# Performance work log

Hardware: AMD Instinct MI355X
Metric: run time of the kernel (lower is better)

Reference implementation:

```python
import jax, jax.numpy as jnp
import numpy as np
from jax import lax

B, C, H, W = 4, 64, 384, 384


def setup_inputs() -> dict:
    key = jax.random.key(0)
    ks = jax.random.split(key, 9)
    s = 1.0 / np.sqrt(C)
    inp = {
        "x": jax.random.normal(ks[0], (B, C, H, W), dtype=jnp.float32),
        "W1": jax.random.normal(ks[1], (C, C), dtype=jnp.float32) * s,
        "b1": jax.random.normal(ks[2], (C,), dtype=jnp.float32) * 0.01,
        "W2": jax.random.normal(ks[3], (C, C), dtype=jnp.float32) * s,
        "b2": jax.random.normal(ks[4], (C,), dtype=jnp.float32) * 0.01,
        "W4": jax.random.normal(ks[5], (C, C), dtype=jnp.float32) * s,
        "b4": jax.random.normal(ks[6], (C,), dtype=jnp.float32) * 0.01,
        "W5": jax.random.normal(ks[7], (C, C), dtype=jnp.float32) * s,
        "b5": jax.random.normal(ks[8], (C,), dtype=jnp.float32) * 0.01,
    }
    return inp


def _lin(Wm, b, t):
    # 1x1 Conv1d == per-position linear: t is (B, C, L)
    return jnp.einsum('oc,bcl->bol', Wm, t) + b[None, :, None]


def reference(x, W1, b1, W2, b2, W4, b4, W5, b5):
    # ---- vertical (top->down) scan over height ----
    rows = jnp.moveaxis(x, 2, 0)          # (H, B, C, W)
    row0 = rows[0]                        # row 0 untouched (no relu in loop 1)

    def vstep(prev, xi):
        new = jax.nn.relu(_lin(W1, b1, xi) + _lin(W2, b2, prev))
        return new, new

    _, vrest = lax.scan(vstep, row0, rows[1:])
    hs = jnp.concatenate([row0[None], vrest], axis=0)   # (H, B, C, W)
    hs = jnp.moveaxis(hs, 0, 2)                          # (B, C, H, W)

    # ---- horizontal (left->right) scan over width ----
    cols = jnp.moveaxis(hs, 3, 0)         # (W, B, C, H)
    col0 = jax.nn.relu(cols[0])           # relu applied to column 0 as well

    def hstep(prev, cj):
        new = jax.nn.relu(_lin(W4, b4, cj) + _lin(W5, b5, prev))
        return new, new

    _, hrest = lax.scan(hstep, col0, cols[1:])
    hse = jnp.concatenate([col0[None], hrest], axis=0)   # (W, B, C, H)
    out = jnp.moveaxis(hse, 0, 3)                        # (B, C, H, W)
    return out
```

## Files before the change

kernel.cpp:

```cpp
#include <hip/hip_runtime.h>


#define C64 64
#define S   384

typedef float v2f __attribute__((ext_vector_type(2)));

static __device__ __forceinline__ v2f mk2(float a, float b) {
    v2f r; r.x = a; r.y = b; return r;
}

#define LOADRB16(SRC)                                                         \
    float4 rb[16];                                                            \
    {                                                                         \
        const float4* vq4_ = (const float4*)(SRC);                            \
        _Pragma("unroll")                                                     \
        for (int i_ = 0; i_ < 16; ++i_) rb[i_] = vq4_[i_];                    \
    }
#define MATVEC16(DST, WREG, INIT)                                             \
    float DST;                                                                \
    {                                                                         \
        v2f a0 = mk2((INIT), 0.f), a1 = mk2(0.f,0.f),                         \
            a2v = mk2(0.f,0.f),    a3 = mk2(0.f,0.f);                         \
        _Pragma("unroll")                                                     \
        for (int i_ = 0; i_ < 8; ++i_) {                                      \
            float4 r0 = rb[2*i_], r1 = rb[2*i_+1];                            \
            a0  = __builtin_elementwise_fma(WREG[4*i_+0], mk2(r0.x,r0.y), a0);\
            a1  = __builtin_elementwise_fma(WREG[4*i_+1], mk2(r0.z,r0.w), a1);\
            a2v = __builtin_elementwise_fma(WREG[4*i_+2], mk2(r1.x,r1.y), a2v);\
            a3  = __builtin_elementwise_fma(WREG[4*i_+3], mk2(r1.z,r1.w), a3);\
        }                                                                     \
        v2f sv = (a0 + a1) + (a2v + a3);                                      \
        DST = sv.x + sv.y;                                                    \
    }

#define MATVEC_H(DST, WREG, SRC, INIT)                                        \
    float DST;                                                                \
    {                                                                         \
        const float4* vq4_ = (const float4*)(SRC);                            \
        v2f a0 = mk2((INIT), 0.f), a1 = mk2(0.f,0.f),                         \
            a2v = mk2(0.f,0.f),    a3 = mk2(0.f,0.f);                         \
        _Pragma("unroll")                                                     \
        for (int h_ = 0; h_ < 2; ++h_) {                                      \
            float4 rb8[8];                                                    \
            _Pragma("unroll")                                                 \
            for (int i_ = 0; i_ < 8; ++i_) rb8[i_] = vq4_[8*h_ + i_];         \
            _Pragma("unroll")                                                 \
            for (int i_ = 0; i_ < 4; ++i_) {                                  \
                float4 r0 = rb8[2*i_], r1 = rb8[2*i_+1];                      \
                a0  = __builtin_elementwise_fma(WREG[16*h_+4*i_+0],           \
                                                mk2(r0.x,r0.y), a0);          \
                a1  = __builtin_elementwise_fma(WREG[16*h_+4*i_+1],           \
                                                mk2(r0.z,r0.w), a1);          \
                a2v = __builtin_elementwise_fma(WREG[16*h_+4*i_+2],           \
                                                mk2(r1.x,r1.y), a2v);         \
                a3  = __builtin_elementwise_fma(WREG[16*h_+4*i_+3],           \
                                                mk2(r1.z,r1.w), a3);          \
            }                                                                 \
        }                                                                     \
        v2f sv = (a0 + a1) + (a2v + a3);                                      \
        DST = sv.x + sv.y;                                                    \
    }

#define LOADW(WSEL)                                                           \
    {                                                                         \
        const float4* P4_ = (const float4*)((WSEL) + o * C64);                \
        _Pragma("unroll")                                                     \
        for (int i_ = 0; i_ < 16; ++i_) {                                     \
            float4 u_ = P4_[i_];                                              \
            wr2[2*i_+0] = mk2(u_.x, u_.y);                                    \
            wr2[2*i_+1] = mk2(u_.z, u_.w);                                    \
        }                                                                     \
        _Pragma("unroll")                                                     \
        for (int i_ = 0; i_ < 32; ++i_) asm volatile("" : "+v"(wr2[i_]));     \
    }

__global__ __launch_bounds__(256, 4)
void prelin_kernel(const float* __restrict__ X, float* __restrict__ A,
                   const float* __restrict__ W, const float* __restrict__ bx,
                   const float* __restrict__ by)
{
    __shared__ float os[C64][68];
    const int p  = blockIdx.x;
    const int q0 = blockIdx.y * 64;
    const int b  = blockIdx.z;
    const int t  = threadIdx.x, wid = t >> 6, l = t & 63;
    const int q  = q0 + l;
    const int o0 = __builtin_amdgcn_readfirstlane(wid * 16);

    if (p == 0) {
        const int tb = ((b * C64 + o0) * S) * S + q;
#pragma unroll
        for (int j = 0; j < 16; ++j)
            os[l][o0 + j] = X[tb + j * S * S];
    } else {
        v2f acc[16];
#pragma unroll
        for (int j = 0; j < 16; ++j) acc[j] = mk2(0.f, 0.f);
#pragma unroll
        for (int cb = 0; cb < 2; ++cb) {
            v2f vin[16];
            const int tb = ((b * C64 + cb * 32) * S + p) * S + q;
#pragma unroll
            for (int i = 0; i < 16; ++i)
                vin[i] = mk2(X[tb + (2*i) * S*S], X[tb + (2*i+1) * S*S]);
#pragma unroll
            for (int j = 0; j < 16; ++j) {
                const v2f* wr = (const v2f*)(W + (o0 + j) * C64 + cb * 32);
#pragma unroll
                for (int i = 0; i < 16; ++i)
                    acc[j] = __builtin_elementwise_fma(wr[i], vin[i], acc[j]);
            }
        }
#pragma unroll
        for (int j = 0; j < 16; ++j)
            os[l][o0 + j] = acc[j].x + acc[j].y + bx[o0 + j] + by[o0 + j];
    }
    __syncthreads();

#pragma unroll
    for (int kk = 0; kk < 4; ++kk) {
        const int qq = 16 * kk + (l >> 2);
        const int oo = 16 * wid + 4 * (l & 3);
        *(float4*)(A + (((b*S + (q0+qq))*S + p) * C64 + oo)) =
            *(const float4*)&os[qq][oo];
    }
}

__global__ __launch_bounds__(64, 2)
void scan1_kernel(const float* __restrict__ A1, float* __restrict__ hsT,
                  const float* __restrict__ W2)
{
    __shared__ float vs[2][C64];
    const int o = threadIdx.x;
    const int g = blockIdx.x, b = g / S, w = g - b * S;

    v2f wr2[32];
    LOADW(W2)

    const int abase = ((b * S + w) * S) * C64 + o;
    const int sb    = (b * S * S + w) * C64 + o;

    float v0 = A1[abase];
    vs[1][o] = v0;
    hsT[sb]  = v0;
    float af[8];
#pragma unroll
    for (int h = 1; h <= 8; ++h) af[h & 7] = A1[abase + h * C64];
    __builtin_amdgcn_wave_barrier();

#define S1STEP(H, PAR)                                                        \
    {                                                                         \
        LOADRB16(&vs[PAR][0])                                                 \
        MATVEC16(s_, wr2, af[(H) & 7])                                        \
        float vnew = fmaxf(s_, 0.0f);                                         \
        vs[(PAR) ^ 1][o] = vnew;                                              \
        hsT[sb + (H) * (S * C64)] = vnew;                                     \
        int hn = (H) + 8; hn = (hn > S - 1) ? (S - 1) : hn;                   \
        af[(H) & 7] = A1[abase + hn * C64];                                   \
        __builtin_amdgcn_wave_barrier();                                      \
    }

    for (int h = 1; h < S - 1; h += 2) { S1STEP(h, 1) S1STEP(h + 1, 0) }
    S1STEP(S - 1, 1)
#undef S1STEP
}

__global__ __launch_bounds__(128, 2)
void scan2_kernel(const float* __restrict__ hsT, float* __restrict__ out,
                  const float* __restrict__ W4, const float* __restrict__ b4,
                  const float* __restrict__ b5, const float* __restrict__ W5)
{
    __shared__ float xr[32][C64];
    __shared__ float xs[2][32][C64];
    __shared__ float vs[2][C64];

    const int t = threadIdx.x, wid = t >> 6, o = t & 63;
    const int g = blockIdx.x, b = g / S, hr = g - b * S;

    const int hbase = ((b * S + hr) * S) * C64 + o;
    const int outb  = ((b * C64 + o) * S + hr) * S;

    v2f wr2[32];
    { const float* Wsel = (wid == 0) ? W5 : W4; LOADW(Wsel) }

    float bias = 0.f;
    if (wid == 1) bias = b4[o] + b5[o];
    if (wid == 0) vs[1][o] = 0.f;
    float ob[16];
    __syncthreads();

    for (int ph = 0; ph < 13; ++ph) {
        if (wid == 1) {
            if (ph < 12) {
                const int k = ph, cb = k & 1, wb = 32 * k;
                float xg[32];
#pragma unroll
                for (int i = 0; i < 32; ++i)
                    xg[i] = hsT[hbase + (wb + i) * C64];
#pragma unroll
                for (int i = 0; i < 32; ++i)
                    xr[i][o] = xg[i];
                __builtin_amdgcn_wave_barrier();
                for (int i = 0; i < 32; ++i) {
                    MATVEC_H(a_, wr2, &xr[i][0], bias)
                    float val = (k == 0 && i == 0) ? xg[0] : a_;
                    xs[cb][i][o] = val;
                }
            }
        } else {
            if (ph >= 1) {
                const int m = ph - 1, cb = m & 1, wb = 32 * m;
                const float* xsrow = &xs[cb][0][0];
#define P2STEP(HALF, I)                                                       \
    {                                                                         \
        MATVEC_H(s_, wr2, &vs[((I) + 1) & 1][0],                              \
                 xsrow[((HALF) * 16 + (I)) * C64 + o])                        \
        float vnew = fmaxf(s_, 0.0f);                                         \
        vs[(I) & 1][o] = vnew;                                                \
        ob[I] = vnew;                                                         \
        __builtin_amdgcn_wave_barrier();                                      \
    }
#define STORE16(BASE)                                                         \
    {                                                                         \
        float4 s0 = {ob[0],  ob[1],  ob[2],  ob[3]};                          \
        float4 s1 = {ob[4],  ob[5],  ob[6],  ob[7]};                          \
        float4 s2 = {ob[8],  ob[9],  ob[10], ob[11]};                         \
        float4 s3 = {ob[12], ob[13], ob[14], ob[15]};                         \
        float4* pp = (float4*)(out + outb + (BASE));                          \
        pp[0] = s0; pp[1] = s1; pp[2] = s2; pp[3] = s3;                       \
    }
                for (int half = 0; half < 2; ++half) {
                    P2STEP(half,  0) P2STEP(half,  1) P2STEP(half,  2)
                    P2STEP(half,  3) P2STEP(half,  4) P2STEP(half,  5)
                    P2STEP(half,  6) P2STEP(half,  7) P2STEP(half,  8)
                    P2STEP(half,  9) P2STEP(half, 10) P2STEP(half, 11)
                    P2STEP(half, 12) P2STEP(half, 13) P2STEP(half, 14)
                    P2STEP(half, 15)
                    STORE16(wb + 16 * half)
                }
#undef P2STEP
#undef STORE16
            }
        }
        __syncthreads();
    }
}

extern "C" void kernel_launch(void* const* d_in, const int* in_sizes, int n_in,
                              void* d_out, int out_size, void* d_ws, size_t ws_size,
                              hipStream_t stream) {
    const float* x  = (const float*)d_in[0];
    const float* W1 = (const float*)d_in[1];
    const float* b1 = (const float*)d_in[2];
    const float* W2 = (const float*)d_in[3];
    const float* b2 = (const float*)d_in[4];
    const float* W4 = (const float*)d_in[5];
    const float* b4 = (const float*)d_in[6];
    const float* W5 = (const float*)d_in[7];
    const float* b5 = (const float*)d_in[8];
    float* out = (float*)d_out;
    float* ws  = (float*)d_ws;

    prelin_kernel<<<dim3(S, 6, 4), dim3(256), 0, stream>>>(x, out, W1, b1, b2);
    scan1_kernel<<<dim3(4 * S), dim3(64), 0, stream>>>(out, ws, W2);
    scan2_kernel<<<dim3(4 * S), dim3(128), 0, stream>>>(ws, out, W4, b4, b5, W5);
}
```

Baseline: 743.3 us.

## Fuse W4 input projection into vertical scan and simplify horizontal scan kernel

The vertical scan kernel now also applies W4 (plus b4+b5) to each new row state, reusing the same LDS-loaded vector for both matvecs, and writes the precomputed horizontal input projection to the workspace. Column 0 keeps the raw relu'd value. The horizontal scan kernel drops its producer/consumer two-wave pipeline with LDS staging and block-wide syncs, becoming a single-wave recurrence that only does the W5 matvec with a 16-deep register prefetch. This takes the W4 matvec off the second kernel's critical path, at the cost of doubling register weight storage and FMA work in the first scan.

```diff
diff --git a/kernel.cpp b/kernel.cpp
--- a/kernel.cpp
+++ b/kernel.cpp
@@ -10,69 +10,17 @@
     v2f r; r.x = a; r.y = b; return r;
 }
 
-#define LOADRB16(SRC)                                                         \
-    float4 rb[16];                                                            \
-    {                                                                         \
-        const float4* vq4_ = (const float4*)(SRC);                            \
-        _Pragma("unroll")                                                     \
-        for (int i_ = 0; i_ < 16; ++i_) rb[i_] = vq4_[i_];                    \
-    }
-#define MATVEC16(DST, WREG, INIT)                                             \
-    float DST;                                                                \
-    {                                                                         \
-        v2f a0 = mk2((INIT), 0.f), a1 = mk2(0.f,0.f),                         \
-            a2v = mk2(0.f,0.f),    a3 = mk2(0.f,0.f);                         \
-        _Pragma("unroll")                                                     \
-        for (int i_ = 0; i_ < 8; ++i_) {                                      \
-            float4 r0 = rb[2*i_], r1 = rb[2*i_+1];                            \
-            a0  = __builtin_elementwise_fma(WREG[4*i_+0], mk2(r0.x,r0.y), a0);\
-            a1  = __builtin_elementwise_fma(WREG[4*i_+1], mk2(r0.z,r0.w), a1);\
-            a2v = __builtin_elementwise_fma(WREG[4*i_+2], mk2(r1.x,r1.y), a2v);\
-            a3  = __builtin_elementwise_fma(WREG[4*i_+3], mk2(r1.z,r1.w), a3);\
-        }                                                                     \
-        v2f sv = (a0 + a1) + (a2v + a3);                                      \
-        DST = sv.x + sv.y;                                                    \
-    }
-
-#define MATVEC_H(DST, WREG, SRC, INIT)                                        \
-    float DST;                                                                \
-    {                                                                         \
-        const float4* vq4_ = (const float4*)(SRC);                            \
-        v2f a0 = mk2((INIT), 0.f), a1 = mk2(0.f,0.f),                         \
-            a2v = mk2(0.f,0.f),    a3 = mk2(0.f,0.f);                         \
-        _Pragma("unroll")                                                     \
-        for (int h_ = 0; h_ < 2; ++h_) {                                      \
-            float4 rb8[8];                                                    \
-            _Pragma("unroll")                                                 \
-            for (int i_ = 0; i_ < 8; ++i_) rb8[i_] = vq4_[8*h_ + i_];         \
-            _Pragma("unroll")                                                 \
-            for (int i_ = 0; i_ < 4; ++i_) {                                  \
-                float4 r0 = rb8[2*i_], r1 = rb8[2*i_+1];                      \
-                a0  = __builtin_elementwise_fma(WREG[16*h_+4*i_+0],           \
-                                                mk2(r0.x,r0.y), a0);          \
-                a1  = __builtin_elementwise_fma(WREG[16*h_+4*i_+1],           \
-                                                mk2(r0.z,r0.w), a1);          \
-                a2v = __builtin_elementwise_fma(WREG[16*h_+4*i_+2],           \
-                                                mk2(r1.x,r1.y), a2v);         \
-                a3  = __builtin_elementwise_fma(WREG[16*h_+4*i_+3],           \
-                                                mk2(r1.z,r1.w), a3);          \
-            }                                                                 \
-        }                                                                     \
-        v2f sv = (a0 + a1) + (a2v + a3);                                      \
-        DST = sv.x + sv.y;                                                    \
-    }
-
-#define LOADW(WSEL)                                                           \
+#define LOADW(DST, WSEL)                                                      \
     {                                                                         \
         const float4* P4_ = (const float4*)((WSEL) + o * C64);                \
         _Pragma("unroll")                                                     \
         for (int i_ = 0; i_ < 16; ++i_) {                                     \
             float4 u_ = P4_[i_];                                              \
-            wr2[2*i_+0] = mk2(u_.x, u_.y);                                    \
-            wr2[2*i_+1] = mk2(u_.z, u_.w);                                    \
-        }                                                                     \
-        _Pragma("unroll")                                                     \
-        for (int i_ = 0; i_ < 32; ++i_) asm volatile("" : "+v"(wr2[i_]));     \
+            DST[2*i_+0] = mk2(u_.x, u_.y);                                    \
+            DST[2*i_+1] = mk2(u_.z, u_.w);                                    \
+        }                                                                     \
+        _Pragma("unroll")                                                     \
+        for (int i_ = 0; i_ < 32; ++i_) asm volatile("" : "+v"(DST[i_]));     \
     }
 
 __global__ __launch_bounds__(256, 4)
@@ -128,99 +76,161 @@
 }
 
 __global__ __launch_bounds__(64, 2)
-void scan1_kernel(const float* __restrict__ A1, float* __restrict__ hsT,
-                  const float* __restrict__ W2)
+void scan1_kernel(const float* __restrict__ A1, float* __restrict__ A2,
+                  const float* __restrict__ W2, const float* __restrict__ W4,
+                  const float* __restrict__ b4, const float* __restrict__ b5)
 {
     __shared__ float vs[2][C64];
     const int o = threadIdx.x;
     const int g = blockIdx.x, b = g / S, w = g - b * S;
-
-    v2f wr2[32];
-    LOADW(W2)
+    const bool w0 = (w == 0);
+
+    v2f w2r[32], w4r[32];
+    LOADW(w2r, W2)
+    LOADW(w4r, W4)
+    const float bias45 = b4[o] + b5[o];
 
     const int abase = ((b * S + w) * S) * C64 + o;
-    const int sb    = (b * S * S + w) * C64 + o;
-
-    float v0 = A1[abase];
-    vs[1][o] = v0;
-    hsT[sb]  = v0;
-    float af[8];
-#pragma unroll
-    for (int h = 1; h <= 8; ++h) af[h & 7] = A1[abase + h * C64];
+    const float* A1p = A1 + abase;
+    float*       A2p = A2 + abase;
+
+    float af[16], ub[16];
+    float v0 = A1p[0];
+    vs[0][o] = v0;
+    float vcur = v0;
+#pragma unroll
+    for (int i = 0; i < 16; ++i) af[i] = A1p[(1 + i) * C64];
     __builtin_amdgcn_wave_barrier();
 
-#define S1STEP(H, PAR)                                                        \
-    {                                                                         \
-        LOADRB16(&vs[PAR][0])                                                 \
-        MATVEC16(s_, wr2, af[(H) & 7])                                        \
-        float vnew = fmaxf(s_, 0.0f);                                         \
-        vs[(PAR) ^ 1][o] = vnew;                                              \
-        hsT[sb + (H) * (S * C64)] = vnew;                                     \
-        int hn = (H) + 8; hn = (hn > S - 1) ? (S - 1) : hn;                   \
-        af[(H) & 7] = A1[abase + hn * C64];                                   \
-        __builtin_amdgcn_wave_barrier();                                      \
-    }
-
-    for (int h = 1; h < S - 1; h += 2) { S1STEP(h, 1) S1STEP(h + 1, 0) }
-    S1STEP(S - 1, 1)
-#undef S1STEP
-}
-
-__global__ __launch_bounds__(128, 2)
-void scan2_kernel(const float* __restrict__ hsT, float* __restrict__ out,
-                  const float* __restrict__ W4, const float* __restrict__ b4,
-                  const float* __restrict__ b5, const float* __restrict__ W5)
+#define SSTEP(H, J, RF)                                                       \
+    {                                                                         \
+        float4 rb[16];                                                        \
+        {                                                                     \
+            const float4* q4_ = (const float4*)&vs[((H) - 1) & 1][0];         \
+            _Pragma("unroll")                                                 \
+            for (int i_ = 0; i_ < 16; ++i_) rb[i_] = q4_[i_];                 \
+        }                                                                     \
+        v2f c0 = mk2(af[J], 0.f),  c1 = mk2(0.f,0.f),                         \
+            c2 = mk2(0.f,0.f),     c3 = mk2(0.f,0.f);                         \
+        v2f d0 = mk2(bias45, 0.f), d1 = mk2(0.f,0.f),                         \
+            d2 = mk2(0.f,0.f),     d3 = mk2(0.f,0.f);                         \
+        _Pragma("unroll")                                                     \
+        for (int i_ = 0; i_ < 8; ++i_) {                                      \
+            float4 r0 = rb[2*i_], r1 = rb[2*i_+1];                            \
+            v2f x0 = mk2(r0.x,r0.y), x1 = mk2(r0.z,r0.w);                     \
+            v2f x2 = mk2(r1.x,r1.y), x3 = mk2(r1.z,r1.w);                     \
+            c0 = __builtin_elementwise_fma(w2r[4*i_+0], x0, c0);              \
+            c1 = __builtin_elementwise_fma(w2r[4*i_+1], x1, c1);              \
+            c2 = __builtin_elementwise_fma(w2r[4*i_+2], x2, c2);              \
+            c3 = __builtin_elementwise_fma(w2r[4*i_+3], x3, c3);              \
+            d0 = __builtin_elementwise_fma(w4r[4*i_+0], x0, d0);              \
+            d1 = __builtin_elementwise_fma(w4r[4*i_+1], x1, d1);              \
+            d2 = __builtin_elementwise_fma(w4r[4*i_+2], x2, d2);              \
+            d3 = __builtin_elementwise_fma(w4r[4*i_+3], x3, d3);              \
+        }                                                                     \
+        v2f sc = (c0 + c1) + (c2 + c3);                                       \
+        v2f sd = (d0 + d1) + (d2 + d3);                                       \
+        ub[J] = w0 ? vcur : (sd.x + sd.y);                                    \
+        float vn_ = fmaxf(sc.x + sc.y, 0.0f);                                 \
+        vs[(H) & 1][o] = vn_;                                                 \
+        vcur = vn_;                                                           \
+        if (RF) {                                                             \
+            int hh = (H) + 16; hh = (hh > S - 1) ? (S - 1) : hh;              \
+            af[J] = A1p[hh * C64];                                            \
+        }                                                                     \
+    }
+
+#define USTORE(H0)                                                            \
+    _Pragma("unroll")                                                         \
+    for (int j_ = 0; j_ < 16; ++j_) A2p[((H0) + j_) * C64] = ub[j_];
+
+    for (int k = 0; k < 23; ++k) {
+        const int h1 = 16 * k + 1;
+        SSTEP(h1+ 0, 0,1) SSTEP(h1+ 1, 1,1) SSTEP(h1+ 2, 2,1)
+        SSTEP(h1+ 3, 3,1) SSTEP(h1+ 4, 4,1) SSTEP(h1+ 5, 5,1)
+        SSTEP(h1+ 6, 6,1) SSTEP(h1+ 7, 7,1) SSTEP(h1+ 8, 8,1)
+        SSTEP(h1+ 9, 9,1) SSTEP(h1+10,10,1) SSTEP(h1+11,11,1)
+        SSTEP(h1+12,12,1) SSTEP(h1+13,13,1) SSTEP(h1+14,14,1)
+        SSTEP(h1+15,15,1)
+        USTORE(16 * k)
+    }
+    SSTEP(369, 0,0) SSTEP(370, 1,0) SSTEP(371, 2,0) SSTEP(372, 3,0)
+    SSTEP(373, 4,0) SSTEP(374, 5,0) SSTEP(375, 6,0) SSTEP(376, 7,0)
+    SSTEP(377, 8,0) SSTEP(378, 9,0) SSTEP(379,10,0) SSTEP(380,11,0)
+    SSTEP(381,12,0) SSTEP(382,13,0) SSTEP(383,14,0)
+    {
+        float4 rb[16];
+        {
+            const float4* q4_ = (const float4*)&vs[1][0];
+#pragma unroll
+            for (int i_ = 0; i_ < 16; ++i_) rb[i_] = q4_[i_];
+        }
+        v2f d0 = mk2(bias45, 0.f), d1 = mk2(0.f,0.f),
+            d2 = mk2(0.f,0.f),     d3 = mk2(0.f,0.f);
+#pragma unroll
+        for (int i_ = 0; i_ < 8; ++i_) {
+            float4 r0 = rb[2*i_], r1 = rb[2*i_+1];
+            d0 = __builtin_elementwise_fma(w4r[4*i_+0], mk2(r0.x,r0.y), d0);
+            d1 = __builtin_elementwise_fma(w4r[4*i_+1], mk2(r0.z,r0.w), d1);
+            d2 = __builtin_elementwise_fma(w4r[4*i_+2], mk2(r1.x,r1.y), d2);
+            d3 = __builtin_elementwise_fma(w4r[4*i_+3], mk2(r1.z,r1.w), d3);
+        }
+        v2f sd = (d0 + d1) + (d2 + d3);
+        ub[15] = w0 ? vcur : (sd.x + sd.y);
+    }
+    USTORE(368)
+#undef SSTEP
+#undef USTORE
+}
+
+__global__ __launch_bounds__(64, 2)
+void scan2_kernel(const float* __restrict__ A2, float* __restrict__ out,
+                  const float* __restrict__ W5)
 {
-    __shared__ float xr[32][C64];
-    __shared__ float xs[2][32][C64];
     __shared__ float vs[2][C64];
-
-    const int t = threadIdx.x, wid = t >> 6, o = t & 63;
+    const int o = threadIdx.x;
     const int g = blockIdx.x, b = g / S, hr = g - b * S;
 
-    const int hbase = ((b * S + hr) * S) * C64 + o;
+    v2f w5r[32];
+    LOADW(w5r, W5)
+
+    const float* A2p = A2 + (b * S * S + hr) * C64 + o;
     const int outb  = ((b * C64 + o) * S + hr) * S;
 
-    v2f wr2[32];
-    { const float* Wsel = (wid == 0) ? W5 : W4; LOADW(Wsel) }
-
-    float bias = 0.f;
-    if (wid == 1) bias = b4[o] + b5[o];
-    if (wid == 0) vs[1][o] = 0.f;
-    float ob[16];
-    __syncthreads();
-
-    for (int ph = 0; ph < 13; ++ph) {
-        if (wid == 1) {
-            if (ph < 12) {
-                const int k = ph, cb = k & 1, wb = 32 * k;
-                float xg[32];
-#pragma unroll
-                for (int i = 0; i < 32; ++i)
-                    xg[i] = hsT[hbase + (wb + i) * C64];
-#pragma unroll
-                for (int i = 0; i < 32; ++i)
-                    xr[i][o] = xg[i];
-                __builtin_amdgcn_wave_barrier();
-                for (int i = 0; i < 32; ++i) {
-                    MATVEC_H(a_, wr2, &xr[i][0], bias)
-                    float val = (k == 0 && i == 0) ? xg[0] : a_;
-                    xs[cb][i][o] = val;
-                }
-            }
-        } else {
-            if (ph >= 1) {
-                const int m = ph - 1, cb = m & 1, wb = 32 * m;
-                const float* xsrow = &xs[cb][0][0];
-#define P2STEP(HALF, I)                                                       \
-    {                                                                         \
-        MATVEC_H(s_, wr2, &vs[((I) + 1) & 1][0],                              \
-                 xsrow[((HALF) * 16 + (I)) * C64 + o])                        \
-        float vnew = fmaxf(s_, 0.0f);                                         \
-        vs[(I) & 1][o] = vnew;                                                \
-        ob[I] = vnew;                                                         \
-        __builtin_amdgcn_wave_barrier();                                      \
-    }
+    float af[16], ob[16];
+    vs[1][o] = 0.f;
+#pragma unroll
+    for (int i = 0; i < 16; ++i) af[i] = A2p[i * (S * C64)];
+    __builtin_amdgcn_wave_barrier();
+
+#define S2STEP(WW, J, RF)                                                     \
+    {                                                                         \
+        float4 rb[16];                                                        \
+        {                                                                     \
+            const float4* q4_ = (const float4*)&vs[((WW) - 1) & 1][0];        \
+            _Pragma("unroll")                                                 \
+            for (int i_ = 0; i_ < 16; ++i_) rb[i_] = q4_[i_];                 \
+        }                                                                     \
+        v2f c0 = mk2(af[J], 0.f), c1 = mk2(0.f,0.f),                          \
+            c2 = mk2(0.f,0.f),    c3 = mk2(0.f,0.f);                          \
+        _Pragma("unroll")                                                     \
+        for (int i_ = 0; i_ < 8; ++i_) {                                      \
+            float4 r0 = rb[2*i_], r1 = rb[2*i_+1];                            \
+            c0 = __builtin_elementwise_fma(w5r[4*i_+0], mk2(r0.x,r0.y), c0);  \
+            c1 = __builtin_elementwise_fma(w5r[4*i_+1], mk2(r0.z,r0.w), c1);  \
+            c2 = __builtin_elementwise_fma(w5r[4*i_+2], mk2(r1.x,r1.y), c2);  \
+            c3 = __builtin_elementwise_fma(w5r[4*i_+3], mk2(r1.z,r1.w), c3);  \
+        }                                                                     \
+        v2f sc = (c0 + c1) + (c2 + c3);                                       \
+        float vn_ = fmaxf(sc.x + sc.y, 0.0f);                                 \
+        vs[(WW) & 1][o] = vn_;                                                \
+        ob[J] = vn_;                                                          \
+        if (RF) {                                                             \
+            int wwn = (WW) + 16; wwn = (wwn > S - 1) ? (S - 1) : wwn;         \
+            af[J] = A2p[wwn * (S * C64)];                                     \
+        }                                                                     \
+    }
+
 #define STORE16(BASE)                                                         \
     {                                                                         \
         float4 s0 = {ob[0],  ob[1],  ob[2],  ob[3]};                          \
@@ -230,21 +240,24 @@
         float4* pp = (float4*)(out + outb + (BASE));                          \
         pp[0] = s0; pp[1] = s1; pp[2] = s2; pp[3] = s3;                       \
     }
-                for (int half = 0; half < 2; ++half) {
-                    P2STEP(half,  0) P2STEP(half,  1) P2STEP(half,  2)
-                    P2STEP(half,  3) P2STEP(half,  4) P2STEP(half,  5)
-                    P2STEP(half,  6) P2STEP(half,  7) P2STEP(half,  8)
-                    P2STEP(half,  9) P2STEP(half, 10) P2STEP(half, 11)
-                    P2STEP(half, 12) P2STEP(half, 13) P2STEP(half, 14)
-                    P2STEP(half, 15)
-                    STORE16(wb + 16 * half)
-                }
-#undef P2STEP
+
+    for (int k = 0; k < 23; ++k) {
+        const int wb = 16 * k;
+        S2STEP(wb+ 0, 0,1) S2STEP(wb+ 1, 1,1) S2STEP(wb+ 2, 2,1)
+        S2STEP(wb+ 3, 3,1) S2STEP(wb+ 4, 4,1) S2STEP(wb+ 5, 5,1)
+        S2STEP(wb+ 6, 6,1) S2STEP(wb+ 7, 7,1) S2STEP(wb+ 8, 8,1)
+        S2STEP(wb+ 9, 9,1) S2STEP(wb+10,10,1) S2STEP(wb+11,11,1)
+        S2STEP(wb+12,12,1) S2STEP(wb+13,13,1) S2STEP(wb+14,14,1)
+        S2STEP(wb+15,15,1)
+        STORE16(wb)
+    }
+    S2STEP(368, 0,0) S2STEP(369, 1,0) S2STEP(370, 2,0) S2STEP(371, 3,0)
+    S2STEP(372, 4,0) S2STEP(373, 5,0) S2STEP(374, 6,0) S2STEP(375, 7,0)
+    S2STEP(376, 8,0) S2STEP(377, 9,0) S2STEP(378,10,0) S2STEP(379,11,0)
+    S2STEP(380,12,0) S2STEP(381,13,0) S2STEP(382,14,0) S2STEP(383,15,0)
+    STORE16(368)
+#undef S2STEP
 #undef STORE16
-            }
-        }
-        __syncthreads();
-    }
 }
 
 extern "C" void kernel_launch(void* const* d_in, const int* in_sizes, int n_in,
@@ -263,6 +276,6 @@
     float* ws  = (float*)d_ws;
 
     prelin_kernel<<<dim3(S, 6, 4), dim3(256), 0, stream>>>(x, out, W1, b1, b2);
-    scan1_kernel<<<dim3(4 * S), dim3(64), 0, stream>>>(out, ws, W2);
-    scan2_kernel<<<dim3(4 * S), dim3(128), 0, stream>>>(ws, out, W4, b4, b5, W5);
-}
+    scan1_kernel<<<dim3(4 * S), dim3(64), 0, stream>>>(out, ws, W2, W4, b4, b5);
+    scan2_kernel<<<dim3(4 * S), dim3(64), 0, stream>>>(ws, out, W5);
+}
```

Measured after the change: 604.2 us. -18.7%, faster.
